# Kernel optimization log

Hardware: AMD Instinct MI355X
Metric: run time of the kernel (lower is better)

The kernel has to match this reference:

```python
import jax, jax.numpy as jnp
import numpy as np

SR = 44100
D = SR * 30          # duration_samples = 1_323_000
N = 1024             # number of note events
L = 32768            # max note length in samples
W = 1024             # hann window length (module's window_length)
H = 8                # harmonics in the synth
K = 128              # FIR taps in the effect chain
LAT = 2              # time_latent_size


def setup_inputs() -> dict:
    key = jax.random.key(0)
    ks = jax.random.split(key, 10)
    freq_rad = jax.random.uniform(ks[0], (N,), jnp.float32, 0.01, 0.3)
    velocity = jax.random.uniform(ks[1], (N,), jnp.float32, 1.0, 127.0)
    starts = jax.random.randint(ks[2], (N,), 0, D - L, dtype=jnp.int32)
    lengths = jax.random.randint(ks[3], (N,), 2048, L + 1, dtype=jnp.int32)
    # time_embedder: Linear(1,32) -> ReLU -> Linear(32,LAT)
    w1 = jax.random.normal(ks[4], (1, 32), jnp.float32)
    b1 = jnp.zeros((32,), jnp.float32)
    w2 = jax.random.normal(ks[5], (32, LAT), jnp.float32) / jnp.sqrt(32.0)
    b2 = jnp.zeros((LAT,), jnp.float32)
    # synth amplitude MLP: [freq, vel, latent] (2+LAT) -> 64 -> H
    ws1 = jax.random.normal(ks[6], (2 + LAT, 64), jnp.float32)
    bs1 = jnp.zeros((64,), jnp.float32)
    ws2 = jax.random.normal(ks[7], (64, H), jnp.float32) / 8.0
    bs2 = jnp.zeros((H,), jnp.float32)
    # effect chain: causal FIR (OIW layout) + tanh
    fir = jax.random.normal(ks[8], (1, 1, K), jnp.float32) / K
    return dict(freq_rad=freq_rad, velocity=velocity,
                w1=w1, b1=b1, w2=w2, b2=b2,
                ws1=ws1, bs1=bs1, ws2=ws2, bs2=bs2, fir=fir,
                starts=starts, lengths=lengths, duration_samples=D)


def reference(freq_rad, velocity, w1, b1, w2, b2, ws1, bs1, ws2, bs2, fir,
              starts, lengths, duration_samples):
    Dn = int(duration_samples)
    t = jnp.arange(L, dtype=jnp.float32)            # [L]
    ti = jnp.arange(L, dtype=jnp.int32)             # [L]
    ends = starts + lengths
    # output_length = min(end, duration) - start, clipped to [0, L]
    out_len = jnp.clip(jnp.minimum(ends, Dn) - starts, 0, L)  # [N]
    # time latent: MLP on normalized start time
    nt = (starts.astype(jnp.float32) / Dn)[:, None]           # [N,1]
    lat = jax.nn.relu(nt @ w1 + b1) @ w2 + b2                  # [N,LAT]
    vel = (velocity / 127.0)[:, None]                          # [N,1]
    # harmonic amplitudes from tiny MLP (the 'synth')
    feat = jnp.concatenate([freq_rad[:, None], vel, lat], axis=-1)  # [N,2+LAT]
    amps = jax.nn.softplus(jax.nn.relu(feat @ ws1 + bs1) @ ws2 + bs2)  # [N,H]
    # additive synthesis; fixed small loop over harmonics, vectorized over [N,L]
    phase = freq_rad[:, None] * t[None, :]                     # [N,L]
    seg = jnp.zeros((N, L), jnp.float32)
    for hh in range(1, H + 1):
        seg = seg + amps[:, hh - 1:hh] * jnp.sin(hh * phase)
    seg = seg * vel
    # hann window (torch periodic) on the LAST W samples of each variable-length segment
    n = jnp.arange(W, dtype=jnp.float32)
    hann = 0.5 * (1.0 - jnp.cos(2.0 * jnp.pi * n / W))         # [W]
    wpos = ti[None, :] - (out_len[:, None] - W)                # [N,L]
    in_win = (wpos >= 0) & (wpos < W)
    factor = jnp.where(in_win, hann[jnp.clip(wpos, 0, W - 1)], 1.0)
    mask = (ti[None, :] < out_len[:, None]).astype(jnp.float32)  # zero past segment end
    seg = seg * factor * mask
    # effect chain: causal 128-tap FIR then tanh (masked so padding stays silent)
    y = jax.lax.conv_general_dilated(seg[:, None, :], fir,
                                     window_strides=(1,), padding=[(K - 1, 0)])
    seg = jnp.tanh(y[:, 0, :]) * mask                          # [N,L]
    # overlap-add: scatter each note into the output buffer
    idx = starts[:, None] + ti[None, :]                        # [N,L]
    valid = (ti[None, :] < out_len[:, None]) & (idx < Dn)
    contrib = jnp.where(valid, seg, 0.0)
    out = jnp.zeros((Dn,), jnp.float32).at[jnp.clip(idx, 0, Dn - 1).reshape(-1)].add(
        contrib.reshape(-1))
    return out
```

## Files before the change

### kernel.cpp

```cpp
#include <hip/hip_runtime.h>
#include <math.h>

#define LMAX  32768
#define WWIN  1024
#define KFIR  128
#define WOUT  256
#define TO    1024
#define SEGX  384
#define CPAD  400
#define NMAX  1024

typedef _Float16 v8h __attribute__((ext_vector_type(8)));
typedef _Float16 v4h __attribute__((ext_vector_type(4)));
typedef float    v4f __attribute__((ext_vector_type(4)));

__global__ __launch_bounds__(256) void params_k(
    const float* __restrict__ freq, const float* __restrict__ velo,
    const float* __restrict__ w1,  const float* __restrict__ b1,
    const float* __restrict__ w2,  const float* __restrict__ b2,
    const float* __restrict__ ws1, const float* __restrict__ bs1,
    const float* __restrict__ ws2, const float* __restrict__ bs2,
    const int* __restrict__ starts, const int* __restrict__ lengths,
    int Dn, int N,
    float* __restrict__ amps_out, int* __restrict__ outlen_out,
    float* __restrict__ veln_out)
{
    __shared__ float s_w1[32], s_b1[32], s_w2[64], s_b2[2];
    __shared__ float s_ws1[256], s_bs1[64], s_ws2[512], s_bs2[8];

    const int tid = threadIdx.x;
    if (tid < 32)  { s_w1[tid] = w1[tid]; s_b1[tid] = b1[tid]; }
    if (tid < 64)  { s_w2[tid] = w2[tid]; s_bs1[tid] = bs1[tid]; }
    if (tid < 2)   s_b2[tid] = b2[tid];
    if (tid < 8)   s_bs2[tid] = bs2[tid];
    s_ws1[tid] = ws1[tid];
    s_ws2[tid] = ws2[tid];
    s_ws2[tid + 256] = ws2[tid + 256];
    __syncthreads();

    const int n = blockIdx.x * blockDim.x + tid;
    if (n >= N) return;

    int st  = starts[n];
    int len = lengths[n];
    int ol  = min(st + len, Dn) - st;
    ol = max(0, min(ol, LMAX));
    outlen_out[n] = ol;

    float v = velo[n] * (1.0f / 127.0f);
    veln_out[n] = v;

    float nt = (float)st / (float)Dn;

    float lat0 = s_b2[0], lat1 = s_b2[1];
    #pragma unroll
    for (int j = 0; j < 32; ++j) {
        float h = fmaxf(fmaf(nt, s_w1[j], s_b1[j]), 0.0f);
        lat0 = fmaf(h, s_w2[j * 2 + 0], lat0);
        lat1 = fmaf(h, s_w2[j * 2 + 1], lat1);
    }

    const float f0 = freq[n], f1 = v, f2 = lat0, f3 = lat1;

    float acc[8];
    #pragma unroll
    for (int h = 0; h < 8; ++h) acc[h] = s_bs2[h];
    #pragma unroll
    for (int j = 0; j < 64; ++j) {
        float a = s_bs1[j];
        a = fmaf(f0, s_ws1[0 * 64 + j], a);
        a = fmaf(f1, s_ws1[1 * 64 + j], a);
        a = fmaf(f2, s_ws1[2 * 64 + j], a);
        a = fmaf(f3, s_ws1[3 * 64 + j], a);
        a = fmaxf(a, 0.0f);
        #pragma unroll
        for (int h = 0; h < 8; ++h)
            acc[h] = fmaf(a, s_ws2[j * 8 + h], acc[h]);
    }
    #pragma unroll
    for (int h = 0; h < 8; ++h) {
        float a = acc[h];
        float sp = fmaxf(a, 0.0f) + log1pf(expf(-fabsf(a)));
        amps_out[n * 8 + h] = sp;
    }
}

__device__ __forceinline__ float fast_tanh(float x) {
    float e = __builtin_amdgcn_exp2f(x * 2.8853900817779268f);
    return fmaf(-2.0f, __builtin_amdgcn_rcpf(e + 1.0f), 1.0f);
}

__global__ __launch_bounds__(256, 3) void synth_gather_k(
    const float* __restrict__ freq_g, const int* __restrict__ starts,
    const float* __restrict__ amps_g, const int* __restrict__ outlen_g,
    const float* __restrict__ veln_g, const float* __restrict__ fir,
    float* __restrict__ out, int Dn, int N)
{
    __shared__ __align__(16) _Float16 segc[4][4][CPAD];
    __shared__ float fir_s[KFIR];
    __shared__ unsigned short note_list[NMAX];
    __shared__ int note_cnt;

    const int tid  = threadIdx.x;
    const int wid  = tid >> 6;
    const int lane = tid & 63;
    const int m    = lane & 15;
    const int quad = lane >> 4;
    const int o0   = blockIdx.x * TO;
    const int o_end = min(o0 + TO, Dn);
    const int ow   = o0 + wid * WOUT;

    if (tid < KFIR) fir_s[tid] = fir[tid];
    if (tid == 0) note_cnt = 0;
    __syncthreads();
    for (int j = tid; j < N; j += 256) {
        int st = starts[j];
        int ol = outlen_g[j];
        if (st < o_end && st + ol > o0) {
            int p = atomicAdd(&note_cnt, 1);
            note_list[p] = (unsigned short)j;
        }
    }
    __syncthreads();
    const int K = note_cnt;

    v8h afrag[12];
    #pragma unroll
    for (int t = 0; t < 12; ++t) {
        v8h af;
        #pragma unroll
        for (int j = 0; j < 8; ++j) {
            int idx = 32 * t + 8 * quad + j - 16 * m;
            float fv = (idx >= 0 && idx < KFIR) ? fir_s[idx] : 0.0f;
            af[j] = (_Float16)fv;
        }
        afrag[t] = af;
    }

    for (int z = lane; z < 4 * 24; z += 64) {
        int S = z / 24, off = z % 24;
        segc[wid][S][376 + off] = (_Float16)0.0f;
    }

    const _Float16* __restrict__ bbase = &segc[wid][m & 3][(m & ~3) + 8 * quad];

    float acc0 = 0.f, acc1 = 0.f, acc2 = 0.f, acc3 = 0.f;

    const double inv2pi = 0.15915494309189535;
    const float4* __restrict__ amps4 = (const float4*)amps_g;

    int stN = 0, olN = 0; float fN = 0.f, vN = 0.f;
    float4 amN0 = {}, amN1 = {};
    if (K > 0) {
        const int nid = __builtin_amdgcn_readfirstlane((int)note_list[0]);
        stN = starts[nid]; olN = outlen_g[nid];
        fN = freq_g[nid];  vN = veln_g[nid];
        amN0 = amps4[nid * 2]; amN1 = amps4[nid * 2 + 1];
    }

    for (int kk = 0; kk < K; ++kk) {
        const int st = stN, ol = olN;
        const float f = fN, v = vN;
        const float4 am0 = amN0, am1 = amN1;
        if (kk + 1 < K) {
            const int nid = __builtin_amdgcn_readfirstlane((int)note_list[kk + 1]);
            stN = starts[nid]; olN = outlen_g[nid];
            fN = freq_g[nid];  vN = veln_g[nid];
            amN0 = amps4[nid * 2]; amN1 = amps4[nid * 2 + 1];
        }

        const int base = ow - st;
        if (base >= ol || base + WOUT <= 0) continue;

        const float A0 = am0.x, A1 = am0.y, A2 = am0.z, A3 = am0.w;
        const float A4 = am1.x, A5 = am1.y, A6 = am1.z, A7 = am1.w;
        const double fd = (double)f;

        const int tseed = base - 127 + lane;
        double rev0 = fd * (double)tseed * inv2pi;
        float r0 = (float)(rev0 - floor(rev0));
        float s = __builtin_amdgcn_sinf(r0);
        float c = __builtin_amdgcn_cosf(r0);
        double d64 = fd * 64.0 * inv2pi;
        float r64 = (float)(d64 - floor(d64));
        const float sd = __builtin_amdgcn_sinf(r64);
        const float cd = __builtin_amdgcn_cosf(r64);
        const int wbase = ol - WWIN;

        #pragma unroll
        for (int i = 0; i < 6; ++i) {
            int t = tseed + 64 * i;
            float val = 0.0f;
            if (t >= 0 && t < ol) {
                float tc = c + c;
                float sA = s;
                float sum = A0 * sA;
                float sB = tc * sA;              sum = fmaf(A1, sB, sum);
                float sC = fmaf(tc, sB, -sA);    sum = fmaf(A2, sC, sum);
                float sD = fmaf(tc, sC, -sB);    sum = fmaf(A3, sD, sum);
                float sE = fmaf(tc, sD, -sC);    sum = fmaf(A4, sE, sum);
                float sF = fmaf(tc, sE, -sD);    sum = fmaf(A5, sF, sum);
                float sG = fmaf(tc, sF, -sE);    sum = fmaf(A6, sG, sum);
                float sH = fmaf(tc, sG, -sF);    sum = fmaf(A7, sH, sum);
                int wpos = t - wbase;
                float factor = 1.0f;
                if (wpos >= 0)
                    factor = 0.5f - 0.5f * __builtin_amdgcn_cosf((float)wpos * (1.0f / WWIN));
                val = v * sum * factor;
            }
            _Float16 h = (_Float16)val;
            const int x = lane + 64 * i;
            if (i == 0) {
                #pragma unroll
                for (int S = 0; S < 4; ++S)
                    if (x >= S) segc[wid][S][x - S] = h;
            } else {
                #pragma unroll
                for (int S = 0; S < 4; ++S)
                    segc[wid][S][x - S] = h;
            }
            float ns = fmaf(s, cd, c * sd);
            float nc = fmaf(c, cd, -(s * sd));
            s = ns; c = nc;
        }

        v4f C0 = {0.f, 0.f, 0.f, 0.f};
        v4f C1 = {0.f, 0.f, 0.f, 0.f};
        #pragma unroll
        for (int t = 0; t < 6; ++t) {
            v4h lo = *(const v4h*)(bbase + 32 * t);
            v4h hi = *(const v4h*)(bbase + 32 * t + 4);
            v8h bf = __builtin_shufflevector(lo, hi, 0, 1, 2, 3, 4, 5, 6, 7);
            C0 = __builtin_amdgcn_mfma_f32_16x16x32_f16(afrag[t], bf, C0, 0, 0, 0);
        }
        #pragma unroll
        for (int t = 6; t < 12; ++t) {
            v4h lo = *(const v4h*)(bbase + 32 * t);
            v4h hi = *(const v4h*)(bbase + 32 * t + 4);
            v8h bf = __builtin_shufflevector(lo, hi, 0, 1, 2, 3, 4, 5, 6, 7);
            C1 = __builtin_amdgcn_mfma_f32_16x16x32_f16(afrag[t], bf, C1, 0, 0, 0);
        }

        {
            const int tb = base + 64 * quad + m;
            float y;
            y = C0[0] + C1[0]; if (tb +  0 >= 0 && tb +  0 < ol) acc0 += fast_tanh(y);
            y = C0[1] + C1[1]; if (tb + 16 >= 0 && tb + 16 < ol) acc1 += fast_tanh(y);
            y = C0[2] + C1[2]; if (tb + 32 >= 0 && tb + 32 < ol) acc2 += fast_tanh(y);
            y = C0[3] + C1[3]; if (tb + 48 >= 0 && tb + 48 < ol) acc3 += fast_tanh(y);
        }
    }

    const int ob = ow + 64 * quad + m;
    if (ob +  0 < Dn) out[ob +  0] = acc0;
    if (ob + 16 < Dn) out[ob + 16] = acc1;
    if (ob + 32 < Dn) out[ob + 32] = acc2;
    if (ob + 48 < Dn) out[ob + 48] = acc3;
}

extern "C" void kernel_launch(void* const* d_in, const int* in_sizes, int n_in,
                              void* d_out, int out_size, void* d_ws, size_t ws_size,
                              hipStream_t stream) {
    const float* freq    = (const float*)d_in[0];
    const float* velo    = (const float*)d_in[1];
    const float* w1      = (const float*)d_in[2];
    const float* b1      = (const float*)d_in[3];
    const float* w2      = (const float*)d_in[4];
    const float* b2      = (const float*)d_in[5];
    const float* ws1     = (const float*)d_in[6];
    const float* bs1     = (const float*)d_in[7];
    const float* ws2     = (const float*)d_in[8];
    const float* bs2     = (const float*)d_in[9];
    const float* fir     = (const float*)d_in[10];
    const int*   starts  = (const int*)d_in[11];
    const int*   lengths = (const int*)d_in[12];

    const int N  = in_sizes[0];
    const int Dn = out_size;
    float* out = (float*)d_out;

    float* amps   = (float*)d_ws;
    int*   outlen = (int*)((char*)d_ws + (size_t)N * 8 * sizeof(float));
    float* veln   = (float*)((char*)d_ws + (size_t)N * 8 * sizeof(float) + (size_t)N * sizeof(int));

    params_k<<<(N + 255) / 256, 256, 0, stream>>>(
        freq, velo, w1, b1, w2, b2, ws1, bs1, ws2, bs2,
        starts, lengths, Dn, N, amps, outlen, veln);

    int n_tiles = (Dn + TO - 1) / TO;
    synth_gather_k<<<n_tiles, 256, 0, stream>>>(
        freq, starts, amps, outlen, veln, fir, out, Dn, N);
}
```

Baseline: 153.9 us.

## Widen per-wave output to 512 samples, fold velocity into amps, add interior fast path

```diff
diff --git a/kernel.cpp b/kernel.cpp
--- a/kernel.cpp
+++ b/kernel.cpp
@@ -4,10 +4,10 @@
 #define LMAX  32768
 #define WWIN  1024
 #define KFIR  128
-#define WOUT  256
+#define WOUT  512
 #define TO    1024
-#define SEGX  384
-#define CPAD  400
+#define SEGX  640
+#define CPAD  656
 #define NMAX  1024
 
 typedef _Float16 v8h __attribute__((ext_vector_type(8)));
@@ -22,8 +22,7 @@
     const float* __restrict__ ws2, const float* __restrict__ bs2,
     const int* __restrict__ starts, const int* __restrict__ lengths,
     int Dn, int N,
-    float* __restrict__ amps_out, int* __restrict__ outlen_out,
-    float* __restrict__ veln_out)
+    float* __restrict__ amps_out, int* __restrict__ outlen_out)
 {
     __shared__ float s_w1[32], s_b1[32], s_w2[64], s_b2[2];
     __shared__ float s_ws1[256], s_bs1[64], s_ws2[512], s_bs2[8];
@@ -48,8 +47,6 @@
     outlen_out[n] = ol;
 
     float v = velo[n] * (1.0f / 127.0f);
-    veln_out[n] = v;
-
     float nt = (float)st / (float)Dn;
 
     float lat0 = s_b2[0], lat1 = s_b2[1];
@@ -81,7 +78,7 @@
     for (int h = 0; h < 8; ++h) {
         float a = acc[h];
         float sp = fmaxf(a, 0.0f) + log1pf(expf(-fabsf(a)));
-        amps_out[n * 8 + h] = sp;
+        amps_out[n * 8 + h] = sp * v;
     }
 }
 
@@ -90,13 +87,13 @@
     return fmaf(-2.0f, __builtin_amdgcn_rcpf(e + 1.0f), 1.0f);
 }
 
-__global__ __launch_bounds__(256, 3) void synth_gather_k(
+__global__ __launch_bounds__(128, 3) void synth_gather_k(
     const float* __restrict__ freq_g, const int* __restrict__ starts,
     const float* __restrict__ amps_g, const int* __restrict__ outlen_g,
-    const float* __restrict__ veln_g, const float* __restrict__ fir,
+    const float* __restrict__ fir,
     float* __restrict__ out, int Dn, int N)
 {
-    __shared__ __align__(16) _Float16 segc[4][4][CPAD];
+    __shared__ __align__(16) _Float16 segc[2][4][CPAD];
     __shared__ float fir_s[KFIR];
     __shared__ unsigned short note_list[NMAX];
     __shared__ int note_cnt;
@@ -110,10 +107,10 @@
     const int o_end = min(o0 + TO, Dn);
     const int ow   = o0 + wid * WOUT;
 
-    if (tid < KFIR) fir_s[tid] = fir[tid];
+    fir_s[tid] = fir[tid];
     if (tid == 0) note_cnt = 0;
     __syncthreads();
-    for (int j = tid; j < N; j += 256) {
+    for (int j = tid; j < N; j += 128) {
         int st = starts[j];
         int ol = outlen_g[j];
         if (st < o_end && st + ol > o0) {
@@ -137,35 +134,36 @@
         afrag[t] = af;
     }
 
-    for (int z = lane; z < 4 * 24; z += 64) {
-        int S = z / 24, off = z % 24;
-        segc[wid][S][376 + off] = (_Float16)0.0f;
+    for (int z = lane; z < 4 * 20; z += 64) {
+        int S = z / 20, off = z % 20;
+        segc[wid][S][636 + off] = (_Float16)0.0f;
     }
 
     const _Float16* __restrict__ bbase = &segc[wid][m & 3][(m & ~3) + 8 * quad];
 
-    float acc0 = 0.f, acc1 = 0.f, acc2 = 0.f, acc3 = 0.f;
+    float accA0 = 0.f, accA1 = 0.f, accA2 = 0.f, accA3 = 0.f;
+    float accB0 = 0.f, accB1 = 0.f, accB2 = 0.f, accB3 = 0.f;
 
     const double inv2pi = 0.15915494309189535;
     const float4* __restrict__ amps4 = (const float4*)amps_g;
 
-    int stN = 0, olN = 0; float fN = 0.f, vN = 0.f;
+    int stN = 0, olN = 0; float fN = 0.f;
     float4 amN0 = {}, amN1 = {};
     if (K > 0) {
         const int nid = __builtin_amdgcn_readfirstlane((int)note_list[0]);
         stN = starts[nid]; olN = outlen_g[nid];
-        fN = freq_g[nid];  vN = veln_g[nid];
+        fN = freq_g[nid];
         amN0 = amps4[nid * 2]; amN1 = amps4[nid * 2 + 1];
     }
 
     for (int kk = 0; kk < K; ++kk) {
         const int st = stN, ol = olN;
-        const float f = fN, v = vN;
+        const float f = fN;
         const float4 am0 = amN0, am1 = amN1;
         if (kk + 1 < K) {
             const int nid = __builtin_amdgcn_readfirstlane((int)note_list[kk + 1]);
             stN = starts[nid]; olN = outlen_g[nid];
-            fN = freq_g[nid];  vN = veln_g[nid];
+            fN = freq_g[nid];
             amN0 = amps4[nid * 2]; amN1 = amps4[nid * 2 + 1];
         }
 
@@ -187,11 +185,11 @@
         const float cd = __builtin_amdgcn_cosf(r64);
         const int wbase = ol - WWIN;
 
-        #pragma unroll
-        for (int i = 0; i < 6; ++i) {
-            int t = tseed + 64 * i;
-            float val = 0.0f;
-            if (t >= 0 && t < ol) {
+        const bool interior = (base >= 127) && (base + 513 <= wbase);
+
+        if (interior) {
+            #pragma unroll
+            for (int i = 0; i < 10; ++i) {
                 float tc = c + c;
                 float sA = s;
                 float sum = A0 * sA;
@@ -202,60 +200,110 @@
                 float sF = fmaf(tc, sE, -sD);    sum = fmaf(A5, sF, sum);
                 float sG = fmaf(tc, sF, -sE);    sum = fmaf(A6, sG, sum);
                 float sH = fmaf(tc, sG, -sF);    sum = fmaf(A7, sH, sum);
-                int wpos = t - wbase;
-                float factor = 1.0f;
-                if (wpos >= 0)
-                    factor = 0.5f - 0.5f * __builtin_amdgcn_cosf((float)wpos * (1.0f / WWIN));
-                val = v * sum * factor;
+                _Float16 h = (_Float16)sum;
+                const int x = lane + 64 * i;
+                if (i == 0) {
+                    #pragma unroll
+                    for (int S = 0; S < 4; ++S)
+                        if (x >= S) segc[wid][S][x - S] = h;
+                } else {
+                    #pragma unroll
+                    for (int S = 0; S < 4; ++S)
+                        segc[wid][S][x - S] = h;
+                }
+                float ns = fmaf(s, cd, c * sd);
+                float nc = fmaf(c, cd, -(s * sd));
+                s = ns; c = nc;
             }
-            _Float16 h = (_Float16)val;
-            const int x = lane + 64 * i;
-            if (i == 0) {
-                #pragma unroll
-                for (int S = 0; S < 4; ++S)
-                    if (x >= S) segc[wid][S][x - S] = h;
-            } else {
-                #pragma unroll
-                for (int S = 0; S < 4; ++S)
-                    segc[wid][S][x - S] = h;
+        } else {
+            #pragma unroll
+            for (int i = 0; i < 10; ++i) {
+                int t = tseed + 64 * i;
+                float val = 0.0f;
+                if (t >= 0 && t < ol) {
+                    float tc = c + c;
+                    float sA = s;
+                    float sum = A0 * sA;
+                    float sB = tc * sA;              sum = fmaf(A1, sB, sum);
+                    float sC = fmaf(tc, sB, -sA);    sum = fmaf(A2, sC, sum);
+                    float sD = fmaf(tc, sC, -sB);    sum = fmaf(A3, sD, sum);
+                    float sE = fmaf(tc, sD, -sC);    sum = fmaf(A4, sE, sum);
+                    float sF = fmaf(tc, sE, -sD);    sum = fmaf(A5, sF, sum);
+                    float sG = fmaf(tc, sF, -sE);    sum = fmaf(A6, sG, sum);
+                    float sH = fmaf(tc, sG, -sF);    sum = fmaf(A7, sH, sum);
+                    int wpos = t - wbase;
+                    float factor = 1.0f;
+                    if (wpos >= 0)
+                        factor = 0.5f - 0.5f * __builtin_amdgcn_cosf((float)wpos * (1.0f / WWIN));
+                    val = sum * factor;
+                }
+                _Float16 h = (_Float16)val;
+                const int x = lane + 64 * i;
+                if (i == 0) {
+                    #pragma unroll
+                    for (int S = 0; S < 4; ++S)
+                        if (x >= S) segc[wid][S][x - S] = h;
+                } else {
+                    #pragma unroll
+                    for (int S = 0; S < 4; ++S)
+                        segc[wid][S][x - S] = h;
+                }
+                float ns = fmaf(s, cd, c * sd);
+                float nc = fmaf(c, cd, -(s * sd));
+                s = ns; c = nc;
             }
-            float ns = fmaf(s, cd, c * sd);
-            float nc = fmaf(c, cd, -(s * sd));
-            s = ns; c = nc;
-        }
-
-        v4f C0 = {0.f, 0.f, 0.f, 0.f};
-        v4f C1 = {0.f, 0.f, 0.f, 0.f};
+        }
+
+        v4f CA0 = {0.f, 0.f, 0.f, 0.f};
+        v4f CA1 = {0.f, 0.f, 0.f, 0.f};
+        v4f CB0 = {0.f, 0.f, 0.f, 0.f};
+        v4f CB1 = {0.f, 0.f, 0.f, 0.f};
         #pragma unroll
         for (int t = 0; t < 6; ++t) {
             v4h lo = *(const v4h*)(bbase + 32 * t);
             v4h hi = *(const v4h*)(bbase + 32 * t + 4);
             v8h bf = __builtin_shufflevector(lo, hi, 0, 1, 2, 3, 4, 5, 6, 7);
-            C0 = __builtin_amdgcn_mfma_f32_16x16x32_f16(afrag[t], bf, C0, 0, 0, 0);
+            CA0 = __builtin_amdgcn_mfma_f32_16x16x32_f16(afrag[t], bf, CA0, 0, 0, 0);
+            v4h lo2 = *(const v4h*)(bbase + 256 + 32 * t);
+            v4h hi2 = *(const v4h*)(bbase + 256 + 32 * t + 4);
+            v8h bf2 = __builtin_shufflevector(lo2, hi2, 0, 1, 2, 3, 4, 5, 6, 7);
+            CB0 = __builtin_amdgcn_mfma_f32_16x16x32_f16(afrag[t], bf2, CB0, 0, 0, 0);
         }
         #pragma unroll
         for (int t = 6; t < 12; ++t) {
             v4h lo = *(const v4h*)(bbase + 32 * t);
             v4h hi = *(const v4h*)(bbase + 32 * t + 4);
             v8h bf = __builtin_shufflevector(lo, hi, 0, 1, 2, 3, 4, 5, 6, 7);
-            C1 = __builtin_amdgcn_mfma_f32_16x16x32_f16(afrag[t], bf, C1, 0, 0, 0);
+            CA1 = __builtin_amdgcn_mfma_f32_16x16x32_f16(afrag[t], bf, CA1, 0, 0, 0);
+            v4h lo2 = *(const v4h*)(bbase + 256 + 32 * t);
+            v4h hi2 = *(const v4h*)(bbase + 256 + 32 * t + 4);
+            v8h bf2 = __builtin_shufflevector(lo2, hi2, 0, 1, 2, 3, 4, 5, 6, 7);
+            CB1 = __builtin_amdgcn_mfma_f32_16x16x32_f16(afrag[t], bf2, CB1, 0, 0, 0);
         }
 
         {
             const int tb = base + 64 * quad + m;
             float y;
-            y = C0[0] + C1[0]; if (tb +  0 >= 0 && tb +  0 < ol) acc0 += fast_tanh(y);
-            y = C0[1] + C1[1]; if (tb + 16 >= 0 && tb + 16 < ol) acc1 += fast_tanh(y);
-            y = C0[2] + C1[2]; if (tb + 32 >= 0 && tb + 32 < ol) acc2 += fast_tanh(y);
-            y = C0[3] + C1[3]; if (tb + 48 >= 0 && tb + 48 < ol) acc3 += fast_tanh(y);
+            y = CA0[0] + CA1[0]; if (tb +   0 >= 0 && tb +   0 < ol) accA0 += fast_tanh(y);
+            y = CA0[1] + CA1[1]; if (tb +  16 >= 0 && tb +  16 < ol) accA1 += fast_tanh(y);
+            y = CA0[2] + CA1[2]; if (tb +  32 >= 0 && tb +  32 < ol) accA2 += fast_tanh(y);
+            y = CA0[3] + CA1[3]; if (tb +  48 >= 0 && tb +  48 < ol) accA3 += fast_tanh(y);
+            y = CB0[0] + CB1[0]; if (tb + 256 >= 0 && tb + 256 < ol) accB0 += fast_tanh(y);
+            y = CB0[1] + CB1[1]; if (tb + 272 >= 0 && tb + 272 < ol) accB1 += fast_tanh(y);
+            y = CB0[2] + CB1[2]; if (tb + 288 >= 0 && tb + 288 < ol) accB2 += fast_tanh(y);
+            y = CB0[3] + CB1[3]; if (tb + 304 >= 0 && tb + 304 < ol) accB3 += fast_tanh(y);
         }
     }
 
     const int ob = ow + 64 * quad + m;
-    if (ob +  0 < Dn) out[ob +  0] = acc0;
-    if (ob + 16 < Dn) out[ob + 16] = acc1;
-    if (ob + 32 < Dn) out[ob + 32] = acc2;
-    if (ob + 48 < Dn) out[ob + 48] = acc3;
+    if (ob +   0 < Dn) out[ob +   0] = accA0;
+    if (ob +  16 < Dn) out[ob +  16] = accA1;
+    if (ob +  32 < Dn) out[ob +  32] = accA2;
+    if (ob +  48 < Dn) out[ob +  48] = accA3;
+    if (ob + 256 < Dn) out[ob + 256] = accB0;
+    if (ob + 272 < Dn) out[ob + 272] = accB1;
+    if (ob + 288 < Dn) out[ob + 288] = accB2;
+    if (ob + 304 < Dn) out[ob + 304] = accB3;
 }
 
 extern "C" void kernel_launch(void* const* d_in, const int* in_sizes, int n_in,
@@ -281,13 +329,12 @@
 
     float* amps   = (float*)d_ws;
     int*   outlen = (int*)((char*)d_ws + (size_t)N * 8 * sizeof(float));
-    float* veln   = (float*)((char*)d_ws + (size_t)N * 8 * sizeof(float) + (size_t)N * sizeof(int));
 
     params_k<<<(N + 255) / 256, 256, 0, stream>>>(
         freq, velo, w1, b1, w2, b2, ws1, bs1, ws2, bs2,
-        starts, lengths, Dn, N, amps, outlen, veln);
+        starts, lengths, Dn, N, amps, outlen);
 
     int n_tiles = (Dn + TO - 1) / TO;
-    synth_gather_k<<<n_tiles, 256, 0, stream>>>(
-        freq, starts, amps, outlen, veln, fir, out, Dn, N);
+    synth_gather_k<<<n_tiles, 128, 0, stream>>>(
+        freq, starts, amps, outlen, fir, out, Dn, N);
 }
```

New measurement: 144.0 us. 1.07x faster.
